# Performance work log

Measured on AMD Instinct MI355X. Metric: run time of the kernel, lower is better.

The kernel has to match this reference:

```python
import jax, jax.numpy as jnp
import numpy as np
import math

DIM = 512
HEADS = 8
DIM_HEAD = DIM // HEADS
TIME_DIM = 512
EPS = 1e-5


def _ln(x, g, b):
    m = jnp.mean(x, axis=-1, keepdims=True)
    v = jnp.var(x, axis=-1, keepdims=True)
    return (x - m) * jax.lax.rsqrt(v + EPS) * g + b


def setup_inputs() -> dict:
    key = jax.random.key(0)
    ks = jax.random.split(key, 16)
    s = 0.02
    return {
        "con_features": jax.random.normal(ks[0], (4, 1024, DIM), jnp.float32),
        "diff_features": jax.random.normal(ks[1], (4, 1024, DIM), jnp.float32),
        "time_emb": jax.random.normal(ks[2], (4, TIME_DIM), jnp.float32),
        "ln_con_g": jnp.ones((DIM,), jnp.float32),
        "ln_con_b": jnp.zeros((DIM,), jnp.float32),
        "ln_diff_g": jnp.ones((DIM,), jnp.float32),
        "ln_diff_b": jnp.zeros((DIM,), jnp.float32),
        "wq": jax.random.normal(ks[3], (DIM, DIM), jnp.float32) * s,
        "wk": jax.random.normal(ks[4], (DIM, DIM), jnp.float32) * s,
        "wv": jax.random.normal(ks[5], (DIM, DIM), jnp.float32) * s,
        "w_out": jax.random.normal(ks[6], (DIM, DIM), jnp.float32) * s,
        "b_out": jnp.zeros((DIM,), jnp.float32),
        "w_emd1": jax.random.normal(ks[7], (TIME_DIM, 2 * DIM), jnp.float32) * s,
        "b_emd1": jnp.zeros((2 * DIM,), jnp.float32),
        "w_emd2": jax.random.normal(ks[8], (2 * DIM, 2 * DIM), jnp.float32) * s,
        "b_emd2": jnp.zeros((2 * DIM,), jnp.float32),
        "mlp_ln_g": jnp.ones((DIM,), jnp.float32),
        "mlp_ln_b": jnp.zeros((DIM,), jnp.float32),
        "mlp_w1": jax.random.normal(ks[9], (DIM, DIM), jnp.float32) * s,
        "mlp_b1": jnp.zeros((DIM,), jnp.float32),
        "mlp_w2": jax.random.normal(ks[10], (DIM, DIM), jnp.float32) * s,
        "mlp_b2": jnp.zeros((DIM,), jnp.float32),
    }


def reference(con_features, diff_features, time_emb,
              ln_con_g, ln_con_b, ln_diff_g, ln_diff_b,
              wq, wk, wv, w_out, b_out,
              w_emd1, b_emd1, w_emd2, b_emd2,
              mlp_ln_g, mlp_ln_b, mlp_w1, mlp_b1, mlp_w2, mlp_b2):
    b, n, _ = diff_features.shape
    fea_q = _ln(diff_features, ln_diff_g, ln_diff_b)
    fea_kv = _ln(con_features, ln_con_g, ln_con_b)
    # projections (no bias) + split heads: b n (h d) -> b h n d
    def heads(x):
        return x.reshape(b, n, HEADS, DIM_HEAD).transpose(0, 2, 1, 3)
    q = heads(fea_q @ wq)
    k = heads(fea_kv @ wk)
    v = heads(fea_kv @ wv)
    # 2D FFT over (n, d), ortho norm
    qf = jnp.fft.fft2(q, axes=(-2, -1), norm="ortho")
    kf = jnp.fft.fft2(k, axes=(-2, -1), norm="ortho")
    dots = jnp.einsum("bhnd,bhmd->bhnm", qf, jnp.conj(kf))  # q @ k^H
    attn_c = jnp.fft.ifft2(dots, axes=(-2, -1), norm="ortho")
    mag = jnp.sqrt(attn_c.real ** 2 + attn_c.imag ** 2)
    attn = jax.nn.softmax(mag, axis=-1) / math.sqrt(DIM_HEAD)
    out = jnp.einsum("bhnm,bhmd->bhnd", attn, v)
    out = out.transpose(0, 2, 1, 3).reshape(b, n, DIM)  # b h n d -> b n (h d)
    # global per-sample normalization over (n, dim); torch.std uses ddof=1
    mu = jnp.mean(out, axis=(-2, -1), keepdims=True)
    sd = jnp.std(out, axis=(-2, -1), keepdims=True, ddof=1)
    out1 = (out - mu) / sd
    # FiLM from time embedding
    t = jax.nn.silu(time_emb @ w_emd1 + b_emd1)
    t = t @ w_emd2 + b_emd2
    mean_t, std_t = jnp.split(t, 2, axis=-1)
    out1 = out1 * std_t[:, None, :] + mean_t[:, None, :]
    out1 = out1 @ w_out + b_out
    # FeedForward: LN -> Linear -> GELU(exact) -> Linear
    h = _ln(out1, mlp_ln_g, mlp_ln_b)
    h = jax.nn.gelu(h @ mlp_w1 + mlp_b1, approximate=False)
    return h @ mlp_w2 + mlp_b2
```

## Files before the change

### kernel.cpp

```cpp
#include <hip/hip_runtime.h>
#include <math.h>


typedef _Float16 f16;
typedef _Float16 f16x4 __attribute__((ext_vector_type(4)));
typedef _Float16 f16x8 __attribute__((ext_vector_type(8)));
typedef float f32x4 __attribute__((ext_vector_type(4)));

#define ROWS 4096
#define NTOK 1024
#define NB   4
#define NH   8
#define DH   64

__device__ __forceinline__ void glds16(const f16* g, f16* l) {
    __builtin_amdgcn_global_load_lds((const __attribute__((address_space(1))) void*)g,
                                     (__attribute__((address_space(3))) void*)l, 16, 0, 0);
}

struct PrepArgs { const float* src[6]; f16* dst[6]; };

__device__ __forceinline__ void ln_row(const float* __restrict__ x, const float* __restrict__ g,
                                       const float* __restrict__ bb, f16* __restrict__ o, int lane) {
    float v[8]; float s = 0.f;
#pragma unroll
    for (int j = 0; j < 8; j++) { v[j] = x[lane + 64 * j]; s += v[j]; }
#pragma unroll
    for (int d = 32; d >= 1; d >>= 1) s += __shfl_xor(s, d, 64);
    float mean = s * (1.f / 512.f);
    float q = 0.f;
#pragma unroll
    for (int j = 0; j < 8; j++) { float t = v[j] - mean; q += t * t; }
#pragma unroll
    for (int d = 32; d >= 1; d >>= 1) q += __shfl_xor(q, d, 64);
    float inv = rsqrtf(q * (1.f / 512.f) + 1e-5f);
#pragma unroll
    for (int j = 0; j < 8; j++) {
        int c = lane + 64 * j;
        o[c] = (f16)((v[j] - mean) * inv * g[c] + bb[c]);
    }
}

__global__ __launch_bounds__(256) void k_pre(PrepArgs pa, float* stats,
                                             const float* __restrict__ b_emd1, const float* __restrict__ b_emd2,
                                             float* __restrict__ tbacc, float* __restrict__ filmp,
                                             float* __restrict__ rstats,
                                             const float* __restrict__ diff, const float* __restrict__ g_dif,
                                             const float* __restrict__ b_dif, f16* __restrict__ A16,
                                             const float* __restrict__ con, const float* __restrict__ g_con,
                                             const float* __restrict__ b_con, f16* __restrict__ C16) {
    __shared__ float smem[1056];
    const int id = blockIdx.x, tid = threadIdx.x;
    if (id < 16) {
        int o = id * 256 + tid;
        tbacc[o] = b_emd1[o & 1023];
        filmp[o] = b_emd2[o & 1023];
        if (id == 0 && tid < 8) stats[tid] = 0.f;
    } else if (id < 48) {
        rstats[(id - 16) * 256 + tid] = 0.f;
    } else if (id < 1584) {
        int pid = id - 48;
        int m = pid >> 8, rem = pid & 255;
        int o0 = (rem & 15) * 32, i0 = (rem >> 4) * 32;
        int tx = tid & 31, ty = tid >> 5;
        const float* src = pa.src[m];
        f16* dst = pa.dst[m];
        for (int r = ty; r < 32; r += 8)
            smem[r * 33 + tx] = src[(i0 + r) * 512 + o0 + tx];
        __syncthreads();
        for (int r = ty; r < 32; r += 8)
            dst[(o0 + r) * 512 + i0 + tx] = (f16)smem[tx * 33 + r];
    } else {
        int lane = tid & 63, wid = tid >> 6;
        long row = (long)(id - 1584) * 4 + wid;
        if (row < ROWS) ln_row(diff + row * 512, g_dif, b_dif, A16 + row * 512, lane);
        else { long r = row - ROWS; ln_row(con + r * 512, g_con, b_con, C16 + r * 512, lane); }
    }
}

__global__ __launch_bounds__(256) void k_qkv(const f16* __restrict__ A16, const f16* __restrict__ C16,
                                             const f16* __restrict__ wqT, const f16* __restrict__ wkT,
                                             const f16* __restrict__ wvT,
                                             f16* __restrict__ Qh, f16* __restrict__ Kf, f16* __restrict__ Vt,
                                             const float* __restrict__ temb, const float* __restrict__ w_emd1,
                                             float* __restrict__ tbacc) {
    __shared__ __attribute__((aligned(16))) f16 sh[128 * 128 + 64 * 128];
    const int id = blockIdx.x, tid = threadIdx.x;
    if (id >= 768) {
        float* tsh = (float*)sh;
        int pid = id - 768;
        int c = (pid & 3) * 256 + tid;
        int k0 = (pid >> 2) * 32;
        if (tid < 128) tsh[(tid >> 5) * 32 + (tid & 31)] = temb[(tid >> 5) * 512 + k0 + (tid & 31)];
        __syncthreads();
        float a0 = 0.f, a1 = 0.f, a2 = 0.f, a3 = 0.f;
#pragma unroll 8
        for (int k = 0; k < 32; k++) {
            float w = w_emd1[(k0 + k) * 1024 + c];
            a0 += tsh[k] * w; a1 += tsh[32 + k] * w; a2 += tsh[64 + k] * w; a3 += tsh[96 + k] * w;
        }
        atomicAdd(&tbacc[c], a0);        atomicAdd(&tbacc[1024 + c], a1);
        atomicAdd(&tbacc[2048 + c], a2); atomicAdd(&tbacc[3072 + c], a3);
        return;
    }
    f16* Ash = sh;
    f16* Bsh = sh + 128 * 128;
    const int z = id >> 8;
    const f16* A  = (z == 0) ? A16 : C16;
    const f16* BT = (z == 0) ? wqT : (z == 1) ? wkT : wvT;
    const int lane = tid & 63, wid = tid >> 6;
    const int quad = lane >> 4, l15 = lane & 15;
    const int m0 = (id & 31) * 128, n0 = ((id >> 5) & 7) * 64;
    const int wm = (wid >> 1) * 64, wn = (wid & 1) * 32;
    const int srow = lane >> 4, slot = lane & 15;
    f32x4 acc[4][2] = {};
    for (int kk = 0; kk < 512; kk += 128) {
        if (kk) __syncthreads();
#pragma unroll
        for (int c = 0; c < 8; c++) {
            int r = c * 16 + 4 * wid + srow;
            int j = slot ^ (r & 7);
            glds16(&A[(long)(m0 + r) * 512 + kk + 8 * j], &Ash[(c * 16 + 4 * wid) * 128]);
        }
#pragma unroll
        for (int c = 0; c < 4; c++) {
            int r = c * 16 + 4 * wid + srow;
            int j = slot ^ (r & 7);
            glds16(&BT[(long)(n0 + r) * 512 + kk + 8 * j], &Bsh[(c * 16 + 4 * wid) * 128]);
        }
        __syncthreads();
#pragma unroll
        for (int ks = 0; ks < 4; ks++) {
            const int rslot = ((ks * 4 + quad) ^ (l15 & 7)) * 8;
            f16x8 af[4], bf[2];
#pragma unroll
            for (int t = 0; t < 4; t++)
                af[t] = *(const f16x8*)&Ash[(wm + t * 16 + l15) * 128 + rslot];
#pragma unroll
            for (int t = 0; t < 2; t++)
                bf[t] = *(const f16x8*)&Bsh[(wn + t * 16 + l15) * 128 + rslot];
#pragma unroll
            for (int mt = 0; mt < 4; mt++)
#pragma unroll
                for (int nt = 0; nt < 2; nt++)
                    acc[mt][nt] = __builtin_amdgcn_mfma_f32_16x16x32_f16(af[mt], bf[nt], acc[mt][nt], 0, 0, 0);
        }
    }
    __syncthreads();
    const int bb = m0 >> 10, nn0 = m0 & 1023, h = (id >> 5) & 7;
    if (z <= 1) {
#pragma unroll
        for (int mt = 0; mt < 4; mt++)
#pragma unroll
            for (int nt = 0; nt < 2; nt++)
#pragma unroll
                for (int r = 0; r < 4; r++)
                    sh[(wm + mt * 16 + quad * 4 + r) * 72 + wn + nt * 16 + l15] = (f16)acc[mt][nt][r];
        __syncthreads();
        f16* dst = (z == 0) ? Qh : Kf;
        long basebh = ((long)(bb * NH + h)) * NTOK * DH;
#pragma unroll
        for (int q2 = 0; q2 < 4; q2++) {
            int c = tid + q2 * 256;
            int row = c >> 3, col = (c & 7) * 8;
            int n = nn0 + row;
            int nr = (z == 1) ? ((NTOK - n) & (NTOK - 1)) : n;
            *(f16x8*)&dst[basebh + (long)nr * DH + col] = *(const f16x8*)&sh[row * 72 + col];
        }
    } else {
#pragma unroll
        for (int mt = 0; mt < 4; mt++)
#pragma unroll
            for (int nt = 0; nt < 2; nt++)
#pragma unroll
                for (int r = 0; r < 4; r++)
                    sh[(wn + nt * 16 + l15) * 136 + wm + mt * 16 + quad * 4 + r] = (f16)acc[mt][nt][r];
        __syncthreads();
        long basev = ((long)(bb * NH + h)) * DH * NTOK;
#pragma unroll
        for (int q2 = 0; q2 < 4; q2++) {
            int c = tid + q2 * 256;
            int d = c >> 4, col = (c & 15) * 8;
            *(f16x8*)&Vt[basev + (long)d * NTOK + nn0 + col] = *(const f16x8*)&sh[d * 136 + col];
        }
    }
}

__global__ __launch_bounds__(256) void k_attn(const f16* __restrict__ Q, const f16* __restrict__ Kf,
                                              const f16* __restrict__ Vt, f16* __restrict__ out,
                                              float* __restrict__ stats,
                                              const float* __restrict__ tbacc, const float* __restrict__ w_emd2,
                                              float* __restrict__ filmp) {
    __shared__ __attribute__((aligned(16))) f16 Ksh[128 * 64];
    __shared__ __attribute__((aligned(16))) f16 Vsh[64 * 128];
    __shared__ __attribute__((aligned(16))) f16 PshT[4 * 32 * 136];
    __shared__ float rbuf[8];
    const int id = blockIdx.x, tid = threadIdx.x;
    if (id >= 256) {
        float* tsh = (float*)Ksh;
        int pid = id - 256;
        int c = (pid & 3) * 256 + tid;
        int k0 = (pid >> 2) * 32;
        if (tid < 128) {
            float v = tbacc[(tid >> 5) * 1024 + k0 + (tid & 31)];
            tsh[(tid >> 5) * 32 + (tid & 31)] = v / (1.f + __expf(-v));
        }
        __syncthreads();
        float a0 = 0.f, a1 = 0.f, a2 = 0.f, a3 = 0.f;
#pragma unroll 8
        for (int k = 0; k < 32; k++) {
            float w = w_emd2[(k0 + k) * 1024 + c];
            a0 += tsh[k] * w; a1 += tsh[32 + k] * w; a2 += tsh[64 + k] * w; a3 += tsh[96 + k] * w;
        }
        atomicAdd(&filmp[c], a0);        atomicAdd(&filmp[1024 + c], a1);
        atomicAdd(&filmp[2048 + c], a2); atomicAdd(&filmp[3072 + c], a3);
        return;
    }
    const int lane = tid & 63, wid = tid >> 6;
    const int quad = lane >> 4, l15 = lane & 15;
    const int bh = id & 31;
    const int b = bh >> 3, hh = bh & 7, q0 = (id >> 5) * 128;
    const f16* Qbh = Q + (long)bh * NTOK * DH;
    const f16* Kbh = Kf + (long)bh * NTOK * DH;
    const f16* Vbh = Vt + (long)bh * DH * NTOK;
    const int rl = lane >> 3, jj8 = (lane & 7) ^ rl;
    const int rl4 = lane >> 4, jjv = (lane & 15) ^ (4 * wid + rl4);
    const int qbase = q0 + wid * 32;
    f16x8 qf[2][2];
#pragma unroll
    for (int h = 0; h < 2; h++) {
        qf[h][0] = *(const f16x8*)&Qbh[(long)(qbase + 16 * h + l15) * DH + quad * 8];
        qf[h][1] = *(const f16x8*)&Qbh[(long)(qbase + 16 * h + l15) * DH + 32 + quad * 8];
    }
    f32x4 O0[4] = {}, O1[4] = {};
    float l0 = 0.f, l1 = 0.f;
    f16* Pw = PshT + wid * 32 * 136;

    for (int k0 = 0; k0 < NTOK; k0 += 128) {
        if (k0) __syncthreads();
#pragma unroll
        for (int c = 0; c < 4; c++) {
            int rk = c * 32 + 8 * wid + rl;
            glds16(&Kbh[(long)(k0 + rk) * DH + 8 * jj8], &Ksh[(c * 32 + 8 * wid) * 64]);
        }
#pragma unroll
        for (int c = 0; c < 4; c++) {
            int rv = c * 16 + 4 * wid + rl4;
            glds16(&Vbh[(long)rv * NTOK + k0 + 8 * jjv], &Vsh[(c * 16 + 4 * wid) * 128]);
        }
        __syncthreads();
        f32x4 st0[8] = {}, st1[8] = {};
#pragma unroll
        for (int ks = 0; ks < 2; ks++) {
            const int slot = ((ks * 4 + quad) ^ (l15 & 7)) * 8;
#pragma unroll
            for (int nt = 0; nt < 8; nt++) {
                f16x8 kf = *(const f16x8*)&Ksh[(nt * 16 + l15) * 64 + slot];
                st0[nt] = __builtin_amdgcn_mfma_f32_16x16x32_f16(kf, qf[0][ks], st0[nt], 0, 0, 0);
                st1[nt] = __builtin_amdgcn_mfma_f32_16x16x32_f16(kf, qf[1][ks], st1[nt], 0, 0, 0);
            }
        }
#pragma unroll
        for (int nt = 0; nt < 8; nt++) {
            float p0 = __expf(fminf(fabsf(st0[nt][0]) - 8.f, 11.f));
            float p1 = __expf(fminf(fabsf(st0[nt][1]) - 8.f, 11.f));
            float p2 = __expf(fminf(fabsf(st0[nt][2]) - 8.f, 11.f));
            float p3 = __expf(fminf(fabsf(st0[nt][3]) - 8.f, 11.f));
            l0 += (p0 + p1) + (p2 + p3);
            f16x4 pk0 = { (f16)p0, (f16)p1, (f16)p2, (f16)p3 };
            *(f16x4*)&Pw[l15 * 136 + 16 * nt + quad * 4] = pk0;
            float u0 = __expf(fminf(fabsf(st1[nt][0]) - 8.f, 11.f));
            float u1 = __expf(fminf(fabsf(st1[nt][1]) - 8.f, 11.f));
            float u2 = __expf(fminf(fabsf(st1[nt][2]) - 8.f, 11.f));
            float u3 = __expf(fminf(fabsf(st1[nt][3]) - 8.f, 11.f));
            l1 += (u0 + u1) + (u2 + u3);
            f16x4 pk1 = { (f16)u0, (f16)u1, (f16)u2, (f16)u3 };
            *(f16x4*)&Pw[(16 + l15) * 136 + 16 * nt + quad * 4] = pk1;
        }
#pragma unroll
        for (int ks = 0; ks < 4; ks++) {
            f16x8 pf0 = *(const f16x8*)&Pw[l15 * 136 + 32 * ks + quad * 8];
            f16x8 pf1 = *(const f16x8*)&Pw[(16 + l15) * 136 + 32 * ks + quad * 8];
            const int vslot = ((ks * 4 + quad) ^ l15) * 8;
#pragma unroll
            for (int vt = 0; vt < 4; vt++) {
                f16x8 vf = *(const f16x8*)&Vsh[(vt * 16 + l15) * 128 + vslot];
                O0[vt] = __builtin_amdgcn_mfma_f32_16x16x32_f16(pf0, vf, O0[vt], 0, 0, 0);
                O1[vt] = __builtin_amdgcn_mfma_f32_16x16x32_f16(pf1, vf, O1[vt], 0, 0, 0);
            }
        }
    }
    l0 += __shfl_xor(l0, 16, 64); l0 += __shfl_xor(l0, 32, 64);
    l1 += __shfl_xor(l1, 16, 64); l1 += __shfl_xor(l1, 32, 64);
    float lb0[4], lb1[4];
#pragma unroll
    for (int r = 0; r < 4; r++) {
        lb0[r] = 0.125f / __shfl(l0, quad * 4 + r, 64);
        lb1[r] = 0.125f / __shfl(l1, quad * 4 + r, 64);
    }
    float lsum = 0.f, lsq = 0.f;
#pragma unroll
    for (int t = 0; t < 4; t++)
#pragma unroll
        for (int r = 0; r < 4; r++) {
            float v0 = O0[t][r] * lb0[r];
            float v1 = O1[t][r] * lb1[r];
            int gc = hh * DH + t * 16 + l15;
            int g0 = qbase + quad * 4 + r;
            int g1 = qbase + 16 + quad * 4 + r;
            out[((long)b * NTOK + g0) * 512 + gc] = (f16)v0;
            out[((long)b * NTOK + g1) * 512 + gc] = (f16)v1;
            lsum += v0 + v1; lsq += v0 * v0 + v1 * v1;
        }
#pragma unroll
    for (int d = 32; d >= 1; d >>= 1) { lsum += __shfl_xor(lsum, d, 64); lsq += __shfl_xor(lsq, d, 64); }
    if (lane == 0) { rbuf[wid] = lsum; rbuf[4 + wid] = lsq; }
    __syncthreads();
    if (tid == 0) {
        atomicAdd(&stats[b * 2], rbuf[0] + rbuf[1] + rbuf[2] + rbuf[3]);
        atomicAdd(&stats[b * 2 + 1], rbuf[4] + rbuf[5] + rbuf[6] + rbuf[7]);
    }
}

__global__ __launch_bounds__(256) void k_gemm2f(const f16* __restrict__ aout16, const float* __restrict__ stats,
                                                const float* __restrict__ filmp,
                                                const f16* __restrict__ BT, const float* __restrict__ bias,
                                                f16* __restrict__ out1h, float* __restrict__ rstats) {
    __shared__ __attribute__((aligned(16))) f16 Ash[64 * 128];
    __shared__ __attribute__((aligned(16))) f16 Bsh[64 * 128];
    __shared__ float scsh[512], shsh[512];
    const int tid = threadIdx.x;
    const int lane = tid & 63, wid = tid >> 6;
    const int quad = lane >> 4, l15 = lane & 15;
    const int m0 = blockIdx.x * 64, n0 = blockIdx.y * 64;
    const int wm = (wid >> 1) * 32, wn = (wid & 1) * 32;
    const int srow = lane >> 4, slot = lane & 15;
    const int b = m0 >> 10;
    {
        float sum = stats[b * 2], sq = stats[b * 2 + 1];
        const float M = 524288.f;
        float mu = sum / M;
        float isd = rsqrtf((sq - sum * mu) / (M - 1.f));
        for (int c = tid; c < 512; c += 256) {
            float sc = isd * filmp[b * 1024 + 512 + c];
            scsh[c] = sc;
            shsh[c] = filmp[b * 1024 + c] - mu * sc;
        }
    }
    __syncthreads();
    f32x4 acc[2][2] = {};
    for (int kk = 0; kk < 512; kk += 128) {
        if (kk) __syncthreads();
        const int j = slot ^ ((4 * wid + srow) & 7);
        const int gcol = kk + 8 * j;
        float sc[8], sf[8];
        *(float4*)&sc[0] = *(const float4*)&scsh[gcol];
        *(float4*)&sc[4] = *(const float4*)&scsh[gcol + 4];
        *(float4*)&sf[0] = *(const float4*)&shsh[gcol];
        *(float4*)&sf[4] = *(const float4*)&shsh[gcol + 4];
#pragma unroll
        for (int c = 0; c < 4; c++) {
            int r = c * 16 + 4 * wid + srow;
            f16x8 v = *(const f16x8*)&aout16[(long)(m0 + r) * 512 + gcol];
            f16x8 y;
#pragma unroll
            for (int e = 0; e < 8; e++) y[e] = (f16)((float)v[e] * sc[e] + sf[e]);
            *(f16x8*)&Ash[(c * 16 + 4 * wid) * 128 + lane * 8] = y;
            glds16(&BT[(long)(n0 + r) * 512 + kk + 8 * j], &Bsh[(c * 16 + 4 * wid) * 128]);
        }
        __syncthreads();
#pragma unroll
        for (int ks = 0; ks < 4; ks++) {
            const int rslot = ((ks * 4 + quad) ^ (l15 & 7)) * 8;
            f16x8 af[2], bf[2];
#pragma unroll
            for (int t = 0; t < 2; t++) {
                af[t] = *(const f16x8*)&Ash[(wm + t * 16 + l15) * 128 + rslot];
                bf[t] = *(const f16x8*)&Bsh[(wn + t * 16 + l15) * 128 + rslot];
            }
#pragma unroll
            for (int mt = 0; mt < 2; mt++)
#pragma unroll
                for (int nt = 0; nt < 2; nt++)
                    acc[mt][nt] = __builtin_amdgcn_mfma_f32_16x16x32_f16(af[mt], bf[nt], acc[mt][nt], 0, 0, 0);
        }
    }
#pragma unroll
    for (int mt = 0; mt < 2; mt++)
#pragma unroll
        for (int r = 0; r < 4; r++) {
            int gm = m0 + wm + mt * 16 + quad * 4 + r;
            float v0 = acc[mt][0][r] + bias[n0 + wn + l15];
            float v1 = acc[mt][1][r] + bias[n0 + wn + 16 + l15];
            out1h[(long)gm * 512 + n0 + wn + l15] = (f16)v0;
            out1h[(long)gm * 512 + n0 + wn + 16 + l15] = (f16)v1;
            float s = v0 + v1, q2 = v0 * v0 + v1 * v1;
#pragma unroll
            for (int d = 8; d >= 1; d >>= 1) { s += __shfl_xor(s, d, 16); q2 += __shfl_xor(q2, d, 16); }
            if (l15 == 0) {
                atomicAdd(&rstats[gm * 2], s);
                atomicAdd(&rstats[gm * 2 + 1], q2);
            }
        }
}

__global__ __launch_bounds__(256) void k_gemm3f(const f16* __restrict__ out1h, const float* __restrict__ rstats,
                                                const float* __restrict__ lng, const float* __restrict__ lnb,
                                                const f16* __restrict__ BT, const float* __restrict__ bias,
                                                f16* __restrict__ X4) {
    __shared__ __attribute__((aligned(16))) f16 Ash[64 * 128];
    __shared__ __attribute__((aligned(16))) f16 Bsh[64 * 128];
    __shared__ float musr[64], invsr[64], gsh[512], bsh[512];
    const int tid = threadIdx.x;
    const int lane = tid & 63, wid = tid >> 6;
    const int quad = lane >> 4, l15 = lane & 15;
    const int m0 = blockIdx.x * 64, n0 = blockIdx.y * 64;
    const int wm = (wid >> 1) * 32, wn = (wid & 1) * 32;
    const int srow = lane >> 4, slot = lane & 15;
    if (tid < 64) {
        float s = rstats[(m0 + tid) * 2], sq = rstats[(m0 + tid) * 2 + 1];
        float mu = s * (1.f / 512.f);
        float var = sq * (1.f / 512.f) - mu * mu;
        musr[tid] = mu;
        invsr[tid] = rsqrtf(var + 1e-5f);
    }
    for (int i = tid; i < 512; i += 256) { gsh[i] = lng[i]; bsh[i] = lnb[i]; }
    __syncthreads();
    f32x4 acc[2][2] = {};
    for (int kk = 0; kk < 512; kk += 128) {
        if (kk) __syncthreads();
        const int j = slot ^ ((4 * wid + srow) & 7);
        const int gcol = kk + 8 * j;
        float gv[8], bv[8];
        *(float4*)&gv[0] = *(const float4*)&gsh[gcol];
        *(float4*)&gv[4] = *(const float4*)&gsh[gcol + 4];
        *(float4*)&bv[0] = *(const float4*)&bsh[gcol];
        *(float4*)&bv[4] = *(const float4*)&bsh[gcol + 4];
#pragma unroll
        for (int c = 0; c < 4; c++) {
            int r = c * 16 + 4 * wid + srow;
            f16x8 x = *(const f16x8*)&out1h[(long)(m0 + r) * 512 + gcol];
            float a = invsr[r], m = musr[r];
            f16x8 y;
#pragma unroll
            for (int e = 0; e < 8; e++) {
                float sc = a * gv[e];
                y[e] = (f16)((float)x[e] * sc + (bv[e] - m * sc));
            }
            *(f16x8*)&Ash[(c * 16 + 4 * wid) * 128 + lane * 8] = y;
            glds16(&BT[(long)(n0 + r) * 512 + kk + 8 * j], &Bsh[(c * 16 + 4 * wid) * 128]);
        }
        __syncthreads();
#pragma unroll
        for (int ks = 0; ks < 4; ks++) {
            const int rslot = ((ks * 4 + quad) ^ (l15 & 7)) * 8;
            f16x8 af[2], bf[2];
#pragma unroll
            for (int t = 0; t < 2; t++) {
                af[t] = *(const f16x8*)&Ash[(wm + t * 16 + l15) * 128 + rslot];
                bf[t] = *(const f16x8*)&Bsh[(wn + t * 16 + l15) * 128 + rslot];
            }
#pragma unroll
            for (int mt = 0; mt < 2; mt++)
#pragma unroll
                for (int nt = 0; nt < 2; nt++)
                    acc[mt][nt] = __builtin_amdgcn_mfma_f32_16x16x32_f16(af[mt], bf[nt], acc[mt][nt], 0, 0, 0);
        }
    }
#pragma unroll
    for (int mt = 0; mt < 2; mt++)
#pragma unroll
        for (int nt = 0; nt < 2; nt++)
#pragma unroll
            for (int r = 0; r < 4; r++) {
                int gm = m0 + wm + mt * 16 + quad * 4 + r;
                int gn = n0 + wn + nt * 16 + l15;
                float x = acc[mt][nt][r] + bias[gn];
                X4[(long)gm * 512 + gn] = (f16)(0.5f * x * (1.0f + erff(x * 0.70710678f)));
            }
}

__global__ __launch_bounds__(256) void k_gemm4(const f16* __restrict__ A, const f16* __restrict__ BT,
                                               const float* __restrict__ bias, float* __restrict__ dst) {
    __shared__ __attribute__((aligned(16))) f16 Ash[64 * 128];
    __shared__ __attribute__((aligned(16))) f16 Bsh[64 * 128];
    const int tid = threadIdx.x;
    const int lane = tid & 63, wid = tid >> 6;
    const int quad = lane >> 4, l15 = lane & 15;
    const int m0 = blockIdx.x * 64, n0 = blockIdx.y * 64;
    const int wm = (wid >> 1) * 32, wn = (wid & 1) * 32;
    const int srow = lane >> 4, slot = lane & 15;
    f32x4 acc[2][2] = {};
    for (int kk = 0; kk < 512; kk += 128) {
        if (kk) __syncthreads();
#pragma unroll
        for (int c = 0; c < 4; c++) {
            int r = c * 16 + 4 * wid + srow;
            int j = slot ^ (r & 7);
            glds16(&A[(long)(m0 + r) * 512 + kk + 8 * j], &Ash[(c * 16 + 4 * wid) * 128]);
            glds16(&BT[(long)(n0 + r) * 512 + kk + 8 * j], &Bsh[(c * 16 + 4 * wid) * 128]);
        }
        __syncthreads();
#pragma unroll
        for (int ks = 0; ks < 4; ks++) {
            const int rslot = ((ks * 4 + quad) ^ (l15 & 7)) * 8;
            f16x8 af[2], bf[2];
#pragma unroll
            for (int t = 0; t < 2; t++) {
                af[t] = *(const f16x8*)&Ash[(wm + t * 16 + l15) * 128 + rslot];
                bf[t] = *(const f16x8*)&Bsh[(wn + t * 16 + l15) * 128 + rslot];
            }
#pragma unroll
            for (int mt = 0; mt < 2; mt++)
#pragma unroll
                for (int nt = 0; nt < 2; nt++)
                    acc[mt][nt] = __builtin_amdgcn_mfma_f32_16x16x32_f16(af[mt], bf[nt], acc[mt][nt], 0, 0, 0);
        }
    }
#pragma unroll
    for (int mt = 0; mt < 2; mt++)
#pragma unroll
        for (int nt = 0; nt < 2; nt++)
#pragma unroll
            for (int r = 0; r < 4; r++) {
                int gm = m0 + wm + mt * 16 + quad * 4 + r;
                int gn = n0 + wn + nt * 16 + l15;
                dst[(long)gm * 512 + gn] = acc[mt][nt][r] + bias[gn];
            }
}

extern "C" void kernel_launch(void* const* d_in, const int* in_sizes, int n_in,
                              void* d_out, int out_size, void* d_ws, size_t ws_size,
                              hipStream_t stream) {
    const float* con      = (const float*)d_in[0];
    const float* diff     = (const float*)d_in[1];
    const float* temb     = (const float*)d_in[2];
    const float* ln_con_g = (const float*)d_in[3];
    const float* ln_con_b = (const float*)d_in[4];
    const float* ln_dif_g = (const float*)d_in[5];
    const float* ln_dif_b = (const float*)d_in[6];
    const float* wq       = (const float*)d_in[7];
    const float* wk       = (const float*)d_in[8];
    const float* wv       = (const float*)d_in[9];
    const float* w_out    = (const float*)d_in[10];
    const float* b_out    = (const float*)d_in[11];
    const float* w_emd1   = (const float*)d_in[12];
    const float* b_emd1   = (const float*)d_in[13];
    const float* w_emd2   = (const float*)d_in[14];
    const float* b_emd2   = (const float*)d_in[15];
    const float* mlp_ln_g = (const float*)d_in[16];
    const float* mlp_ln_b = (const float*)d_in[17];
    const float* mlp_w1   = (const float*)d_in[18];
    const float* mlp_b1   = (const float*)d_in[19];
    const float* mlp_w2   = (const float*)d_in[20];
    const float* mlp_b2   = (const float*)d_in[21];
    float* outp = (float*)d_out;

    char* ws = (char*)d_ws;
    size_t off = 0;
    auto alloc = [&](size_t bytes) { void* p = ws + off; off += (bytes + 255) & ~(size_t)255; return p; };
    f16*   A16   = (f16*)alloc((size_t)ROWS * 512 * 2);
    f16*   C16   = (f16*)alloc((size_t)ROWS * 512 * 2);
    f16*   Qh    = (f16*)alloc((size_t)ROWS * 512 * 2);
    f16*   Kf    = (f16*)alloc((size_t)ROWS * 512 * 2);
    f16*   Vt    = (f16*)alloc((size_t)ROWS * 512 * 2);
    f16*   aout16= (f16*)alloc((size_t)ROWS * 512 * 2);
    f16*   wqT   = (f16*)alloc(512 * 512 * 2);
    f16*   wkT   = (f16*)alloc(512 * 512 * 2);
    f16*   wvT   = (f16*)alloc(512 * 512 * 2);
    f16*   woT   = (f16*)alloc(512 * 512 * 2);
    f16*   w1T   = (f16*)alloc(512 * 512 * 2);
    f16*   w2T   = (f16*)alloc(512 * 512 * 2);
    float* tbacc = (float*)alloc(4 * 1024 * 4);
    float* filmp = (float*)alloc(4 * 1024 * 4);
    float* stats = (float*)alloc(256);
    float* rstats= (float*)alloc(ROWS * 2 * 4);
    f16*   out1h = Qh;
    f16*   X4    = C16;

    PrepArgs pa;
    pa.src[0] = wq;  pa.src[1] = wk;  pa.src[2] = wv;
    pa.src[3] = w_out; pa.src[4] = mlp_w1; pa.src[5] = mlp_w2;
    pa.dst[0] = wqT; pa.dst[1] = wkT; pa.dst[2] = wvT;
    pa.dst[3] = woT; pa.dst[4] = w1T; pa.dst[5] = w2T;

    k_pre<<<dim3(3632), dim3(256), 0, stream>>>(pa, stats, b_emd1, b_emd2, tbacc, filmp, rstats,
                                                diff, ln_dif_g, ln_dif_b, A16,
                                                con, ln_con_g, ln_con_b, C16);
    k_qkv<<<dim3(832), dim3(256), 0, stream>>>(A16, C16, wqT, wkT, wvT, Qh, Kf, Vt,
                                               temb, w_emd1, tbacc);
    k_attn<<<dim3(384), dim3(256), 0, stream>>>(Qh, Kf, Vt, aout16, stats,
                                                tbacc, w_emd2, filmp);
    k_gemm2f<<<dim3(64, 8), dim3(256), 0, stream>>>(aout16, stats, filmp, woT, b_out, out1h, rstats);
    k_gemm3f<<<dim3(64, 8), dim3(256), 0, stream>>>(out1h, rstats, mlp_ln_g, mlp_ln_b, w1T, mlp_b1, X4);
    k_gemm4<<<dim3(64, 8), dim3(256), 0, stream>>>(X4, w2T, mlp_b2, outp);
}
```

Before: 186.8 us.

## Split attention over key halves with partial results and a combine kernel

```diff
diff --git a/kernel.cpp b/kernel.cpp
--- a/kernel.cpp
+++ b/kernel.cpp
@@ -187,18 +187,100 @@
 }
 
 __global__ __launch_bounds__(256) void k_attn(const f16* __restrict__ Q, const f16* __restrict__ Kf,
-                                              const f16* __restrict__ Vt, f16* __restrict__ out,
-                                              float* __restrict__ stats,
+                                              const f16* __restrict__ Vt,
+                                              float* __restrict__ Opart, float* __restrict__ lpart) {
+    __shared__ __attribute__((aligned(16))) f16 Ksh[128 * 64];
+    __shared__ __attribute__((aligned(16))) f16 Vsh[64 * 128];
+    __shared__ __attribute__((aligned(16))) f16 PshT[4 * 16 * 136];
+    const int id = blockIdx.x, tid = threadIdx.x;
+    const int lane = tid & 63, wid = tid >> 6;
+    const int quad = lane >> 4, l15 = lane & 15;
+    const int bh = id & 31;
+    const int rest = id >> 5;
+    const int qt = rest & 15, half = rest >> 4;
+    const int b = bh >> 3, hh = bh & 7, q0 = qt * 64;
+    const int kbase = half * 512;
+    const f16* Qbh = Q + (long)bh * NTOK * DH;
+    const f16* Kbh = Kf + (long)bh * NTOK * DH;
+    const f16* Vbh = Vt + (long)bh * DH * NTOK;
+    const int rl = lane >> 3, jj8 = (lane & 7) ^ rl;
+    const int rl4 = lane >> 4, jjv = (lane & 15) ^ (4 * wid + rl4);
+    const int qrow = q0 + wid * 16 + l15;
+    f16x8 qf[2];
+    qf[0] = *(const f16x8*)&Qbh[(long)qrow * DH + quad * 8];
+    qf[1] = *(const f16x8*)&Qbh[(long)qrow * DH + 32 + quad * 8];
+    f32x4 O[4] = {};
+    float l_acc = 0.f;
+    f16* Pw = PshT + wid * 16 * 136;
+
+    for (int k0 = 0; k0 < 512; k0 += 128) {
+        if (k0) __syncthreads();
+        const int kb = kbase + k0;
+#pragma unroll
+        for (int c = 0; c < 4; c++) {
+            int rk = c * 32 + 8 * wid + rl;
+            glds16(&Kbh[(long)(kb + rk) * DH + 8 * jj8], &Ksh[(c * 32 + 8 * wid) * 64]);
+        }
+#pragma unroll
+        for (int c = 0; c < 4; c++) {
+            int rv = c * 16 + 4 * wid + rl4;
+            glds16(&Vbh[(long)rv * NTOK + kb + 8 * jjv], &Vsh[(c * 16 + 4 * wid) * 128]);
+        }
+        __syncthreads();
+        f32x4 st[8] = {};
+#pragma unroll
+        for (int ks = 0; ks < 2; ks++) {
+            const int slot = ((ks * 4 + quad) ^ (l15 & 7)) * 8;
+#pragma unroll
+            for (int nt = 0; nt < 8; nt++) {
+                f16x8 kf = *(const f16x8*)&Ksh[(nt * 16 + l15) * 64 + slot];
+                st[nt] = __builtin_amdgcn_mfma_f32_16x16x32_f16(kf, qf[ks], st[nt], 0, 0, 0);
+            }
+        }
+#pragma unroll
+        for (int nt = 0; nt < 8; nt++) {
+            float p0 = __expf(fminf(fabsf(st[nt][0]) - 8.f, 11.f));
+            float p1 = __expf(fminf(fabsf(st[nt][1]) - 8.f, 11.f));
+            float p2 = __expf(fminf(fabsf(st[nt][2]) - 8.f, 11.f));
+            float p3 = __expf(fminf(fabsf(st[nt][3]) - 8.f, 11.f));
+            l_acc += (p0 + p1) + (p2 + p3);
+            f16x4 pk = { (f16)p0, (f16)p1, (f16)p2, (f16)p3 };
+            *(f16x4*)&Pw[l15 * 136 + 16 * nt + quad * 4] = pk;
+        }
+#pragma unroll
+        for (int ks = 0; ks < 4; ks++) {
+            f16x8 pf = *(const f16x8*)&Pw[l15 * 136 + 32 * ks + quad * 8];
+            const int vslot = ((ks * 4 + quad) ^ l15) * 8;
+#pragma unroll
+            for (int vt = 0; vt < 4; vt++) {
+                f16x8 vf = *(const f16x8*)&Vsh[(vt * 16 + l15) * 128 + vslot];
+                O[vt] = __builtin_amdgcn_mfma_f32_16x16x32_f16(pf, vf, O[vt], 0, 0, 0);
+            }
+        }
+    }
+    l_acc += __shfl_xor(l_acc, 16, 64);
+    l_acc += __shfl_xor(l_acc, 32, 64);
+    if (quad == 0) lpart[half * (32 * NTOK) + bh * NTOK + qrow] = l_acc;
+    float* Od = Opart + (size_t)half * ROWS * 512;
+#pragma unroll
+    for (int t = 0; t < 4; t++)
+#pragma unroll
+        for (int r = 0; r < 4; r++) {
+            int gn = q0 + wid * 16 + quad * 4 + r;
+            int gc = hh * DH + t * 16 + l15;
+            Od[((long)b * NTOK + gn) * 512 + gc] = O[t][r];
+        }
+}
+
+__global__ __launch_bounds__(256) void k_comb(const float* __restrict__ Opart, const float* __restrict__ lpart,
+                                              f16* __restrict__ aout16, float* __restrict__ stats,
                                               const float* __restrict__ tbacc, const float* __restrict__ w_emd2,
                                               float* __restrict__ filmp) {
-    __shared__ __attribute__((aligned(16))) f16 Ksh[128 * 64];
-    __shared__ __attribute__((aligned(16))) f16 Vsh[64 * 128];
-    __shared__ __attribute__((aligned(16))) f16 PshT[4 * 32 * 136];
+    __shared__ float tsh[128];
     __shared__ float rbuf[8];
     const int id = blockIdx.x, tid = threadIdx.x;
-    if (id >= 256) {
-        float* tsh = (float*)Ksh;
-        int pid = id - 256;
+    if (id >= 2048) {
+        int pid = id - 2048;
         int c = (pid & 3) * 256 + tid;
         int k0 = (pid >> 2) * 32;
         if (tid < 128) {
@@ -217,101 +299,22 @@
         return;
     }
     const int lane = tid & 63, wid = tid >> 6;
-    const int quad = lane >> 4, l15 = lane & 15;
-    const int bh = id & 31;
-    const int b = bh >> 3, hh = bh & 7, q0 = (id >> 5) * 128;
-    const f16* Qbh = Q + (long)bh * NTOK * DH;
-    const f16* Kbh = Kf + (long)bh * NTOK * DH;
-    const f16* Vbh = Vt + (long)bh * DH * NTOK;
-    const int rl = lane >> 3, jj8 = (lane & 7) ^ rl;
-    const int rl4 = lane >> 4, jjv = (lane & 15) ^ (4 * wid + rl4);
-    const int qbase = q0 + wid * 32;
-    f16x8 qf[2][2];
-#pragma unroll
-    for (int h = 0; h < 2; h++) {
-        qf[h][0] = *(const f16x8*)&Qbh[(long)(qbase + 16 * h + l15) * DH + quad * 8];
-        qf[h][1] = *(const f16x8*)&Qbh[(long)(qbase + 16 * h + l15) * DH + 32 + quad * 8];
-    }
-    f32x4 O0[4] = {}, O1[4] = {};
-    float l0 = 0.f, l1 = 0.f;
-    f16* Pw = PshT + wid * 32 * 136;
-
-    for (int k0 = 0; k0 < NTOK; k0 += 128) {
-        if (k0) __syncthreads();
-#pragma unroll
-        for (int c = 0; c < 4; c++) {
-            int rk = c * 32 + 8 * wid + rl;
-            glds16(&Kbh[(long)(k0 + rk) * DH + 8 * jj8], &Ksh[(c * 32 + 8 * wid) * 64]);
-        }
-#pragma unroll
-        for (int c = 0; c < 4; c++) {
-            int rv = c * 16 + 4 * wid + rl4;
-            glds16(&Vbh[(long)rv * NTOK + k0 + 8 * jjv], &Vsh[(c * 16 + 4 * wid) * 128]);
-        }
-        __syncthreads();
-        f32x4 st0[8] = {}, st1[8] = {};
-#pragma unroll
-        for (int ks = 0; ks < 2; ks++) {
-            const int slot = ((ks * 4 + quad) ^ (l15 & 7)) * 8;
-#pragma unroll
-            for (int nt = 0; nt < 8; nt++) {
-                f16x8 kf = *(const f16x8*)&Ksh[(nt * 16 + l15) * 64 + slot];
-                st0[nt] = __builtin_amdgcn_mfma_f32_16x16x32_f16(kf, qf[0][ks], st0[nt], 0, 0, 0);
-                st1[nt] = __builtin_amdgcn_mfma_f32_16x16x32_f16(kf, qf[1][ks], st1[nt], 0, 0, 0);
-            }
-        }
-#pragma unroll
-        for (int nt = 0; nt < 8; nt++) {
-            float p0 = __expf(fminf(fabsf(st0[nt][0]) - 8.f, 11.f));
-            float p1 = __expf(fminf(fabsf(st0[nt][1]) - 8.f, 11.f));
-            float p2 = __expf(fminf(fabsf(st0[nt][2]) - 8.f, 11.f));
-            float p3 = __expf(fminf(fabsf(st0[nt][3]) - 8.f, 11.f));
-            l0 += (p0 + p1) + (p2 + p3);
-            f16x4 pk0 = { (f16)p0, (f16)p1, (f16)p2, (f16)p3 };
-            *(f16x4*)&Pw[l15 * 136 + 16 * nt + quad * 4] = pk0;
-            float u0 = __expf(fminf(fabsf(st1[nt][0]) - 8.f, 11.f));
-            float u1 = __expf(fminf(fabsf(st1[nt][1]) - 8.f, 11.f));
-            float u2 = __expf(fminf(fabsf(st1[nt][2]) - 8.f, 11.f));
-            float u3 = __expf(fminf(fabsf(st1[nt][3]) - 8.f, 11.f));
-            l1 += (u0 + u1) + (u2 + u3);
-            f16x4 pk1 = { (f16)u0, (f16)u1, (f16)u2, (f16)u3 };
-            *(f16x4*)&Pw[(16 + l15) * 136 + 16 * nt + quad * 4] = pk1;
-        }
-#pragma unroll
-        for (int ks = 0; ks < 4; ks++) {
-            f16x8 pf0 = *(const f16x8*)&Pw[l15 * 136 + 32 * ks + quad * 8];
-            f16x8 pf1 = *(const f16x8*)&Pw[(16 + l15) * 136 + 32 * ks + quad * 8];
-            const int vslot = ((ks * 4 + quad) ^ l15) * 8;
-#pragma unroll
-            for (int vt = 0; vt < 4; vt++) {
-                f16x8 vf = *(const f16x8*)&Vsh[(vt * 16 + l15) * 128 + vslot];
-                O0[vt] = __builtin_amdgcn_mfma_f32_16x16x32_f16(pf0, vf, O0[vt], 0, 0, 0);
-                O1[vt] = __builtin_amdgcn_mfma_f32_16x16x32_f16(pf1, vf, O1[vt], 0, 0, 0);
-            }
-        }
-    }
-    l0 += __shfl_xor(l0, 16, 64); l0 += __shfl_xor(l0, 32, 64);
-    l1 += __shfl_xor(l1, 16, 64); l1 += __shfl_xor(l1, 32, 64);
-    float lb0[4], lb1[4];
-#pragma unroll
-    for (int r = 0; r < 4; r++) {
-        lb0[r] = 0.125f / __shfl(l0, quad * 4 + r, 64);
-        lb1[r] = 0.125f / __shfl(l1, quad * 4 + r, 64);
-    }
-    float lsum = 0.f, lsq = 0.f;
-#pragma unroll
-    for (int t = 0; t < 4; t++)
-#pragma unroll
-        for (int r = 0; r < 4; r++) {
-            float v0 = O0[t][r] * lb0[r];
-            float v1 = O1[t][r] * lb1[r];
-            int gc = hh * DH + t * 16 + l15;
-            int g0 = qbase + quad * 4 + r;
-            int g1 = qbase + 16 + quad * 4 + r;
-            out[((long)b * NTOK + g0) * 512 + gc] = (f16)v0;
-            out[((long)b * NTOK + g1) * 512 + gc] = (f16)v1;
-            lsum += v0 + v1; lsq += v0 * v0 + v1 * v1;
-        }
+    long base = ((long)id * 256 + tid) * 4;
+    int b = (int)(base >> 19);
+    int row = (int)(base >> 9);
+    int n = row & 1023;
+    int col = (int)(base & 511);
+    int h = col >> 6;
+    int bhn = (b * 8 + h) * NTOK + n;
+    float4 o0 = *(const float4*)&Opart[base];
+    float4 o1 = *(const float4*)&Opart[(size_t)ROWS * 512 + base];
+    float fr = 0.125f / (lpart[bhn] + lpart[32 * NTOK + bhn]);
+    float v0 = (o0.x + o1.x) * fr, v1 = (o0.y + o1.y) * fr;
+    float v2 = (o0.z + o1.z) * fr, v3 = (o0.w + o1.w) * fr;
+    f16x4 pk = { (f16)v0, (f16)v1, (f16)v2, (f16)v3 };
+    *(f16x4*)&aout16[base] = pk;
+    float lsum = (v0 + v1) + (v2 + v3);
+    float lsq = (v0 * v0 + v1 * v1) + (v2 * v2 + v3 * v3);
 #pragma unroll
     for (int d = 32; d >= 1; d >>= 1) { lsum += __shfl_xor(lsum, d, 64); lsq += __shfl_xor(lsq, d, 64); }
     if (lane == 0) { rbuf[wid] = lsum; rbuf[4 + wid] = lsq; }
@@ -565,6 +568,8 @@
     f16*   Kf    = (f16*)alloc((size_t)ROWS * 512 * 2);
     f16*   Vt    = (f16*)alloc((size_t)ROWS * 512 * 2);
     f16*   aout16= (f16*)alloc((size_t)ROWS * 512 * 2);
+    float* Opart = (float*)alloc((size_t)2 * ROWS * 512 * 4);
+    float* lpart = (float*)alloc((size_t)2 * 32 * NTOK * 4);
     f16*   wqT   = (f16*)alloc(512 * 512 * 2);
     f16*   wkT   = (f16*)alloc(512 * 512 * 2);
     f16*   wvT   = (f16*)alloc(512 * 512 * 2);
@@ -589,8 +594,9 @@
                                                 con, ln_con_g, ln_con_b, C16);
     k_qkv<<<dim3(832), dim3(256), 0, stream>>>(A16, C16, wqT, wkT, wvT, Qh, Kf, Vt,
                                                temb, w_emd1, tbacc);
-    k_attn<<<dim3(384), dim3(256), 0, stream>>>(Qh, Kf, Vt, aout16, stats,
-                                                tbacc, w_emd2, filmp);
+    k_attn<<<dim3(1024), dim3(256), 0, stream>>>(Qh, Kf, Vt, Opart, lpart);
+    k_comb<<<dim3(2176), dim3(256), 0, stream>>>(Opart, lpart, aout16, stats,
+                                                 tbacc, w_emd2, filmp);
     k_gemm2f<<<dim3(64, 8), dim3(256), 0, stream>>>(aout16, stats, filmp, woT, b_out, out1h, rstats);
     k_gemm3f<<<dim3(64, 8), dim3(256), 0, stream>>>(out1h, rstats, mlp_ln_g, mlp_ln_b, w1T, mlp_b1, X4);
     k_gemm4<<<dim3(64, 8), dim3(256), 0, stream>>>(X4, w2T, mlp_b2, outp);
```

New measurement: 234.8 us. +25.7%, slower.
